# Kernel optimization log

Measured on AMD Instinct MI355X. Metric: run time of the kernel, lower is better.

## Reference

```python
import jax, jax.numpy as jnp
import numpy as np

D_K = 64
MASK_FILL = -1e9


def setup_inputs() -> dict:
    key = jax.random.key(0)
    kq, kk, kv, km = jax.random.split(key, 4)
    B, H, S, D = 2, 16, 2048, D_K
    q = jax.random.normal(kq, (B, H, S, D), dtype=jnp.float32)
    k = jax.random.normal(kk, (B, H, D, S), dtype=jnp.float32)  # pre-transposed keys
    v = jax.random.normal(kv, (B, H, S, D), dtype=jnp.float32)
    mask = jax.random.randint(km, (B, H, S, S), 0, 2).astype(jnp.bool_)
    return {"q": q, "k": k, "v": v, "mask": mask}


def reference(q, k, v, mask):
    # scores: [B, H, S, S] = q @ k (k already [B,H,D,S])
    scores = jnp.einsum("bhsd,bhdt->bhst", q, k) / jnp.sqrt(jnp.float32(D_K))
    scores = jnp.where(mask, MASK_FILL, scores)
    attn = jax.nn.softmax(scores, axis=-1)
    context = jnp.einsum("bhst,bhtd->bhsd", attn, v)
    return (context, attn)
```

## Files before the change

### kernel.cpp

```cpp
#include <hip/hip_runtime.h>

#define S_LEN    2048
#define DK       64
#define N_BH     32
#define ROWS     16
#define NTHREADS 512

typedef float          f32x4  __attribute__((ext_vector_type(4)));
typedef int            i32x4  __attribute__((ext_vector_type(4)));
typedef short          bf16x8 __attribute__((ext_vector_type(8)));
typedef unsigned short u16x8  __attribute__((ext_vector_type(8)));
typedef unsigned int   u32x4  __attribute__((ext_vector_type(4)));

__device__ __forceinline__ unsigned short f2bf(float f) {
    unsigned u = __builtin_bit_cast(unsigned, f);
    u += 0x7fffu + ((u >> 16) & 1u);
    return (unsigned short)(u >> 16);
}
__device__ __forceinline__ float bf2f(unsigned short h) {
    unsigned u = ((unsigned)h) << 16;
    return __builtin_bit_cast(float, u);
}
__device__ __forceinline__ unsigned pack_bf2(float a, float b) {
    return (unsigned)f2bf(a) | ((unsigned)f2bf(b) << 16);
}

__global__ void prep_qcast(const float* __restrict__ q, unsigned short* __restrict__ Qb) {
    const long i = ((long)blockIdx.x * 256 + threadIdx.x) * 8;
    f32x4 a = *(const f32x4*)(q + i);
    f32x4 b = *(const f32x4*)(q + i + 4);
    u16x8 o;
    o[0]=f2bf(a.x); o[1]=f2bf(a.y); o[2]=f2bf(a.z); o[3]=f2bf(a.w);
    o[4]=f2bf(b.x); o[5]=f2bf(b.y); o[6]=f2bf(b.z); o[7]=f2bf(b.w);
    *(u16x8*)(Qb + i) = o;
}

__global__ void prep_k(const float* __restrict__ k, unsigned short* __restrict__ Kb) {
    __shared__ float t[64][65];
    const int bh = blockIdx.x >> 5, s0 = (blockIdx.x & 31) << 6;
    const int tx = threadIdx.x;
    const float* kb = k + (long)bh * 64 * S_LEN;
    #pragma unroll
    for (int i = 0; i < 16; ++i) {
        const int d = (i << 2) + (tx >> 6), s = tx & 63;
        t[d][s] = kb[(long)d * S_LEN + s0 + s];
    }
    __syncthreads();
    #pragma unroll
    for (int i = 0; i < 16; ++i) {
        const int s = (i << 2) + (tx >> 6), d = tx & 63;
        Kb[((long)bh * S_LEN + s0 + s) * DK + d] = f2bf(t[d][s]);
    }
}

__global__ void prep_v(const float* __restrict__ v, unsigned short* __restrict__ Vb) {
    __shared__ float t[64][65];
    const int bh = blockIdx.x >> 5, s0 = (blockIdx.x & 31) << 6;
    const int tx = threadIdx.x;
    #pragma unroll
    for (int i = 0; i < 16; ++i) {
        const int s = (i << 2) + (tx >> 6), d = tx & 63;
        t[s][d] = v[((long)bh * S_LEN + s0 + s) * DK + d];
    }
    __syncthreads();
    #pragma unroll
    for (int i = 0; i < 16; ++i) {
        const int d = (i << 2) + (tx >> 6), s = tx & 63;
        Vb[((long)bh * DK + d) * S_LEN + s0 + s] = f2bf(t[s][d]);
    }
}

template <bool WS>
__global__ __launch_bounds__(NTHREADS, 4)
void sdpa_main(const float* __restrict__ q, const float* __restrict__ k,
               const float* __restrict__ v, const int* __restrict__ mask,
               const unsigned short* __restrict__ Qb,
               const unsigned short* __restrict__ Kb,
               const unsigned short* __restrict__ Vb,
               float* __restrict__ ctx, float* __restrict__ attn)
{
    __shared__ float rowsum[ROWS];
    __shared__ float ctxlds[ROWS * DK];

    const int bid  = blockIdx.x;
    const int bh   = bid & (N_BH - 1);
    const int qt   = bid >> 5;
    const int tid  = threadIdx.x;
    const int wave = tid >> 6;
    const int lane = tid & 63;
    const int m    = lane & 15;
    const int g    = lane >> 4;
    const long rowbase = (long)bh * S_LEN + qt * ROWS;
    const int tw   = wave << 8;

    if (tid < ROWS) rowsum[tid] = 0.0f;
    for (int i = tid; i < ROWS * DK; i += NTHREADS) ctxlds[i] = 0.0f;
    __syncthreads();

    unsigned long long mbits = 0ull;
    {
        const int* mbase = mask + rowbase * S_LEN + tw + 4 * lane;
        #pragma unroll
        for (int r = 0; r < 16; ++r) {
            const i32x4 mk = __builtin_nontemporal_load((const i32x4*)(mbase + (long)r * S_LEN));
            const unsigned nib = (mk.x ? 1u : 0u) | (mk.y ? 2u : 0u)
                               | (mk.z ? 4u : 0u) | (mk.w ? 8u : 0u);
            mbits |= ((unsigned long long)nib) << (r * 4);
        }
    }

    bf16x8 qfrag[2];
    if (WS) {
        const unsigned short* qp = Qb + (rowbase + m) * DK;
        qfrag[0] = *(const bf16x8*)(qp + g * 8);
        qfrag[1] = *(const bf16x8*)(qp + 32 + g * 8);
    } else {
        const float* qp = q + (rowbase + m) * DK;
        #pragma unroll
        for (int ks = 0; ks < 2; ++ks) {
            const float* p = qp + ks * 32 + g * 8;
            f32x4 x0 = *(const f32x4*)p, x1 = *(const f32x4*)(p + 4);
            qfrag[ks][0]=(short)f2bf(x0.x); qfrag[ks][1]=(short)f2bf(x0.y);
            qfrag[ks][2]=(short)f2bf(x0.z); qfrag[ks][3]=(short)f2bf(x0.w);
            qfrag[ks][4]=(short)f2bf(x1.x); qfrag[ks][5]=(short)f2bf(x1.y);
            qfrag[ks][6]=(short)f2bf(x1.z); qfrag[ks][7]=(short)f2bf(x1.w);
        }
    }

    unsigned long long lanemask = 0ull;
    {
        const unsigned mlo = (unsigned)mbits, mhi = (unsigned)(mbits >> 32);
        #pragma unroll
        for (int kt = 0; kt < 8; ++kt) {
            const int sA = kt * 8 + g * 2, sB = sA + 1;
            const unsigned aLo = (unsigned)__shfl((int)mlo, sA);
            const unsigned aHi = (unsigned)__shfl((int)mhi, sA);
            const unsigned bLo = (unsigned)__shfl((int)mlo, sB);
            const unsigned bHi = (unsigned)__shfl((int)mhi, sB);
            const unsigned long long A = ((unsigned long long)aHi << 32) | aLo;
            const unsigned long long B = ((unsigned long long)bHi << 32) | bLo;
            const unsigned byt = (unsigned)((A >> (4 * m)) & 0xFull)
                               | ((unsigned)((B >> (4 * m)) & 0xFull) << 4);
            lanemask |= ((unsigned long long)byt) << (8 * kt);
        }
    }

    const int srcA = ((g & 1) << 5) + m;
    const int srcB = srcA + 16;
    const int hi   = g >> 1;

    u32x4 AF[8];
    f32x4 cacc0 = {0,0,0,0}, cacc1 = {0,0,0,0}, cacc2 = {0,0,0,0}, cacc3 = {0,0,0,0};
    float rsum = 0.0f;

    #pragma unroll
    for (int kt = 0; kt < 8; ++kt) {
        unsigned pk0e, pk1e, pk0o, pk1o;
        #pragma unroll
        for (int h = 0; h < 2; ++h) {
            const int t0 = tw + ((2 * kt + h) << 4);
            const int tk = t0 + m;
            f32x4 acc = {0.f, 0.f, 0.f, 0.f};
            #pragma unroll
            for (int ks = 0; ks < 2; ++ks) {
                bf16x8 kfrag;
                if (WS) {
                    kfrag = *(const bf16x8*)(Kb + ((long)bh * S_LEN + tk) * DK + ks * 32 + g * 8);
                } else {
                    const float* kp = k + (long)bh * DK * S_LEN + (long)(ks * 32 + g * 8) * S_LEN + tk;
                    #pragma unroll
                    for (int j = 0; j < 8; ++j) kfrag[j] = (short)f2bf(kp[(long)j * S_LEN]);
                }
                acc = __builtin_amdgcn_mfma_f32_16x16x32_bf16(kfrag, qfrag[ks], acc, 0, 0, 0);
            }
            const float e0 = __expf(acc[0] * 0.125f);
            const float e1 = __expf(acc[1] * 0.125f);
            const float e2 = __expf(acc[2] * 0.125f);
            const float e3 = __expf(acc[3] * 0.125f);
            if (h == 0) { pk0e = pack_bf2(e0, e1); pk1e = pack_bf2(e2, e3); }
            else        { pk0o = pack_bf2(e0, e1); pk1o = pack_bf2(e2, e3); }
        }
        const unsigned a0e = (unsigned)__shfl((int)pk0e, srcA);
        const unsigned a0o = (unsigned)__shfl((int)pk0o, srcA);
        const unsigned a1e = (unsigned)__shfl((int)pk1e, srcA);
        const unsigned a1o = (unsigned)__shfl((int)pk1o, srcA);
        const unsigned a2e = (unsigned)__shfl((int)pk0e, srcB);
        const unsigned a2o = (unsigned)__shfl((int)pk0o, srcB);
        const unsigned a3e = (unsigned)__shfl((int)pk1e, srcB);
        const unsigned a3o = (unsigned)__shfl((int)pk1o, srcB);
        u32x4 wv = { hi ? a0o : a0e, hi ? a1o : a1e,
                     hi ? a2o : a2e, hi ? a3o : a3e };
        const unsigned mb = (unsigned)(lanemask >> (8 * kt)) & 0xFFu;
        if (mb & 1u)   wv.x &= 0xFFFF0000u;
        if (mb & 2u)   wv.x &= 0x0000FFFFu;
        if (mb & 4u)   wv.y &= 0xFFFF0000u;
        if (mb & 8u)   wv.y &= 0x0000FFFFu;
        if (mb & 16u)  wv.z &= 0xFFFF0000u;
        if (mb & 32u)  wv.z &= 0x0000FFFFu;
        if (mb & 64u)  wv.w &= 0xFFFF0000u;
        if (mb & 128u) wv.w &= 0x0000FFFFu;
        AF[kt] = wv;
        rsum += ((bf2f((unsigned short)(wv.x & 0xFFFF)) + bf2f((unsigned short)(wv.x >> 16)))
               + (bf2f((unsigned short)(wv.y & 0xFFFF)) + bf2f((unsigned short)(wv.y >> 16))))
              + ((bf2f((unsigned short)(wv.z & 0xFFFF)) + bf2f((unsigned short)(wv.z >> 16)))
               + (bf2f((unsigned short)(wv.w & 0xFFFF)) + bf2f((unsigned short)(wv.w >> 16))));
        const bf16x8 af = __builtin_bit_cast(bf16x8, wv);
        const int tb = tw + (kt << 5) + (g << 3);
        #pragma unroll
        for (int dt = 0; dt < 4; ++dt) {
            bf16x8 bfv;
            if (WS) {
                bfv = *(const bf16x8*)(Vb + ((long)bh * DK + dt * 16 + m) * S_LEN + tb);
            } else {
                const float* vp = v + ((long)bh * S_LEN + tb) * DK + dt * 16 + m;
                #pragma unroll
                for (int j = 0; j < 8; ++j) bfv[j] = (short)f2bf(vp[j * DK]);
            }
            if      (dt == 0) cacc0 = __builtin_amdgcn_mfma_f32_16x16x32_bf16(af, bfv, cacc0, 0, 0, 0);
            else if (dt == 1) cacc1 = __builtin_amdgcn_mfma_f32_16x16x32_bf16(af, bfv, cacc1, 0, 0, 0);
            else if (dt == 2) cacc2 = __builtin_amdgcn_mfma_f32_16x16x32_bf16(af, bfv, cacc2, 0, 0, 0);
            else              cacc3 = __builtin_amdgcn_mfma_f32_16x16x32_bf16(af, bfv, cacc3, 0, 0, 0);
        }
    }

    rsum += __shfl_xor(rsum, 16);
    rsum += __shfl_xor(rsum, 32);
    if (lane < 16) atomicAdd(&rowsum[lane], rsum);
    #pragma unroll
    for (int i = 0; i < 4; ++i) {
        atomicAdd(&ctxlds[(4 * g + i) * DK +  0 + m], cacc0[i]);
        atomicAdd(&ctxlds[(4 * g + i) * DK + 16 + m], cacc1[i]);
        atomicAdd(&ctxlds[(4 * g + i) * DK + 32 + m], cacc2[i]);
        atomicAdd(&ctxlds[(4 * g + i) * DK + 48 + m], cacc3[i]);
    }
    __syncthreads();

    {
        const float rinv = 1.0f / rowsum[m];
        float* aout = attn + (rowbase + m) * (long)S_LEN;
        #pragma unroll
        for (int kt = 0; kt < 8; ++kt) {
            const u32x4 wv = AF[kt];
            const int tb = tw + (kt << 5) + (g << 3);
            f32x4 o0 = { bf2f((unsigned short)(wv.x & 0xFFFF)) * rinv,
                         bf2f((unsigned short)(wv.x >> 16))    * rinv,
                         bf2f((unsigned short)(wv.y & 0xFFFF)) * rinv,
                         bf2f((unsigned short)(wv.y >> 16))    * rinv };
            f32x4 o1 = { bf2f((unsigned short)(wv.z & 0xFFFF)) * rinv,
                         bf2f((unsigned short)(wv.z >> 16))    * rinv,
                         bf2f((unsigned short)(wv.w & 0xFFFF)) * rinv,
                         bf2f((unsigned short)(wv.w >> 16))    * rinv };
            __builtin_nontemporal_store(o0, (f32x4*)(aout + tb));
            __builtin_nontemporal_store(o1, (f32x4*)(aout + tb + 4));
        }
    }

    #pragma unroll
    for (int i = tid; i < ROWS * DK; i += NTHREADS) {
        const int rr = i >> 6, dd = i & 63;
        ctx[(rowbase + rr) * DK + dd] = ctxlds[i] / rowsum[rr];
    }
}

extern "C" void kernel_launch(void* const* d_in, const int* in_sizes, int n_in,
                              void* d_out, int out_size, void* d_ws, size_t ws_size,
                              hipStream_t stream)
{
    const float* q    = (const float*)d_in[0];
    const float* k    = (const float*)d_in[1];
    const float* v    = (const float*)d_in[2];
    const int*   mask = (const int*)d_in[3];

    float* ctx  = (float*)d_out;
    float* attn = ctx + (size_t)N_BH * S_LEN * DK;

    const size_t nel = (size_t)N_BH * S_LEN * DK;
    const bool use_ws = ws_size >= nel * 3 * sizeof(unsigned short);
    unsigned short* Qb = (unsigned short*)d_ws;
    unsigned short* Kb = Qb + nel;
    unsigned short* Vb = Kb + nel;

    const int nblocks = N_BH * (S_LEN / ROWS);

    if (use_ws) {
        prep_qcast<<<(int)(nel / (256 * 8)), 256, 0, stream>>>(q, Qb);
        prep_k<<<N_BH * (S_LEN / 64), 256, 0, stream>>>(k, Kb);
        prep_v<<<N_BH * (S_LEN / 64), 256, 0, stream>>>(v, Vb);
        sdpa_main<true><<<nblocks, NTHREADS, 0, stream>>>(q, k, v, mask, Qb, Kb, Vb, ctx, attn);
    } else {
        sdpa_main<false><<<nblocks, NTHREADS, 0, stream>>>(q, k, v, mask,
                                                           nullptr, nullptr, nullptr, ctx, attn);
    }
}
```

Baseline: 475.9 us.

## Pre-swizzle Q/K/V bf16 into MFMA fragment order for contiguous wave loads

The prep kernels now write the bf16 copies of Q, K and V in the exact per-lane fragment order the MFMA instructions consume, so each wave's fragment load becomes one contiguous 1 KB read (lane*8 offset). Before, the main kernel used strided row loads, and the V^T layout was read with an S_LEN stride. This targets memory coalescing and address arithmetic in the main attention loop. The prep kernels get more complex, with vectorised 16-byte stores built from gathered LDS reads.

```diff
diff --git a/kernel.cpp b/kernel.cpp
--- a/kernel.cpp
+++ b/kernel.cpp
@@ -25,21 +25,24 @@
     return (unsigned)f2bf(a) | ((unsigned)f2bf(b) << 16);
 }
 
-__global__ void prep_qcast(const float* __restrict__ q, unsigned short* __restrict__ Qb) {
-    const long i = ((long)blockIdx.x * 256 + threadIdx.x) * 8;
-    f32x4 a = *(const f32x4*)(q + i);
-    f32x4 b = *(const f32x4*)(q + i + 4);
+__global__ void prep_q(const float* __restrict__ q, unsigned short* __restrict__ Q2) {
+    const int bq = blockIdx.x;
+    const int tx = threadIdx.x;
+    const int ks = tx >> 6, g = (tx >> 4) & 3, m = tx & 15;
+    const long row = ((long)(bq >> 7) * S_LEN + (bq & 127) * 16 + m);
+    const float* p = q + row * DK + ks * 32 + g * 8;
+    f32x4 x0 = *(const f32x4*)p, x1 = *(const f32x4*)(p + 4);
     u16x8 o;
-    o[0]=f2bf(a.x); o[1]=f2bf(a.y); o[2]=f2bf(a.z); o[3]=f2bf(a.w);
-    o[4]=f2bf(b.x); o[5]=f2bf(b.y); o[6]=f2bf(b.z); o[7]=f2bf(b.w);
-    *(u16x8*)(Qb + i) = o;
-}
-
-__global__ void prep_k(const float* __restrict__ k, unsigned short* __restrict__ Kb) {
+    o[0]=f2bf(x0.x); o[1]=f2bf(x0.y); o[2]=f2bf(x0.z); o[3]=f2bf(x0.w);
+    o[4]=f2bf(x1.x); o[5]=f2bf(x1.y); o[6]=f2bf(x1.z); o[7]=f2bf(x1.w);
+    *(u16x8*)(Q2 + (long)bq * 1024 + tx * 8) = o;
+}
+
+__global__ void prep_k(const float* __restrict__ k, unsigned short* __restrict__ K2) {
     __shared__ float t[64][65];
     const int bh = blockIdx.x >> 5, s0 = (blockIdx.x & 31) << 6;
     const int tx = threadIdx.x;
-    const float* kb = k + (long)bh * 64 * S_LEN;
+    const float* kb = k + (long)bh * DK * S_LEN;
     #pragma unroll
     for (int i = 0; i < 16; ++i) {
         const int d = (i << 2) + (tx >> 6), s = tx & 63;
@@ -47,13 +50,20 @@
     }
     __syncthreads();
     #pragma unroll
-    for (int i = 0; i < 16; ++i) {
-        const int s = (i << 2) + (tx >> 6), d = tx & 63;
-        Kb[((long)bh * S_LEN + s0 + s) * DK + d] = f2bf(t[d][s]);
-    }
-}
-
-__global__ void prep_v(const float* __restrict__ v, unsigned short* __restrict__ Vb) {
+    for (int it = 0; it < 2; ++it) {
+        const int flat = it * 256 + tx;
+        const int m = flat & 15, g = (flat >> 4) & 3, ks = (flat >> 6) & 1, t16g = flat >> 7;
+        const int sl = t16g * 16 + m;
+        const int d0 = ks * 32 + g * 8;
+        u16x8 o;
+        #pragma unroll
+        for (int j = 0; j < 8; ++j) o[j] = f2bf(t[d0 + j][sl]);
+        const long idx = ((((long)(bh * 128 + (s0 >> 4) + t16g) * 2 + ks) * 4 + g) * 16 + m) * 8;
+        *(u16x8*)(K2 + idx) = o;
+    }
+}
+
+__global__ void prep_v(const float* __restrict__ v, unsigned short* __restrict__ V2) {
     __shared__ float t[64][65];
     const int bh = blockIdx.x >> 5, s0 = (blockIdx.x & 31) << 6;
     const int tx = threadIdx.x;
@@ -64,9 +74,14 @@
     }
     __syncthreads();
     #pragma unroll
-    for (int i = 0; i < 16; ++i) {
-        const int d = (i << 2) + (tx >> 6), s = tx & 63;
-        Vb[((long)bh * DK + d) * S_LEN + s0 + s] = f2bf(t[s][d]);
+    for (int it = 0; it < 2; ++it) {
+        const int flat = it * 256 + tx;
+        const int d = flat & 63, tbl = flat >> 6;
+        u16x8 o;
+        #pragma unroll
+        for (int j = 0; j < 8; ++j) o[j] = f2bf(t[tbl * 8 + j][d]);
+        const long idx = (((long)(bh * 256 + (s0 >> 3) + tbl) * 64) + d) * 8;
+        *(u16x8*)(V2 + idx) = o;
     }
 }
 
@@ -74,9 +89,9 @@
 __global__ __launch_bounds__(NTHREADS, 4)
 void sdpa_main(const float* __restrict__ q, const float* __restrict__ k,
                const float* __restrict__ v, const int* __restrict__ mask,
-               const unsigned short* __restrict__ Qb,
-               const unsigned short* __restrict__ Kb,
-               const unsigned short* __restrict__ Vb,
+               const unsigned short* __restrict__ Q2,
+               const unsigned short* __restrict__ K2,
+               const unsigned short* __restrict__ V2,
                float* __restrict__ ctx, float* __restrict__ attn)
 {
     __shared__ float rowsum[ROWS];
@@ -111,9 +126,9 @@
 
     bf16x8 qfrag[2];
     if (WS) {
-        const unsigned short* qp = Qb + (rowbase + m) * DK;
-        qfrag[0] = *(const bf16x8*)(qp + g * 8);
-        qfrag[1] = *(const bf16x8*)(qp + 32 + g * 8);
+        const unsigned short* qp = Q2 + ((long)((bh * 128 + qt) * 2) << 9) + (lane << 3);
+        qfrag[0] = *(const bf16x8*)qp;
+        qfrag[1] = *(const bf16x8*)(qp + 512);
     } else {
         const float* qp = q + (rowbase + m) * DK;
         #pragma unroll
@@ -158,15 +173,18 @@
         unsigned pk0e, pk1e, pk0o, pk1o;
         #pragma unroll
         for (int h = 0; h < 2; ++h) {
-            const int t0 = tw + ((2 * kt + h) << 4);
-            const int tk = t0 + m;
             f32x4 acc = {0.f, 0.f, 0.f, 0.f};
             #pragma unroll
             for (int ks = 0; ks < 2; ++ks) {
                 bf16x8 kfrag;
                 if (WS) {
-                    kfrag = *(const bf16x8*)(Kb + ((long)bh * S_LEN + tk) * DK + ks * 32 + g * 8);
+                    const unsigned short* kp = K2
+                        + (((long)(bh * 128 + wave * 16 + 2 * kt + h) * 2 + ks) << 9)
+                        + (lane << 3);
+                    kfrag = *(const bf16x8*)kp;
                 } else {
+                    const int t0 = tw + ((2 * kt + h) << 4);
+                    const int tk = t0 + m;
                     const float* kp = k + (long)bh * DK * S_LEN + (long)(ks * 32 + g * 8) * S_LEN + tk;
                     #pragma unroll
                     for (int j = 0; j < 8; ++j) kfrag[j] = (short)f2bf(kp[(long)j * S_LEN]);
@@ -205,13 +223,15 @@
               + ((bf2f((unsigned short)(wv.z & 0xFFFF)) + bf2f((unsigned short)(wv.z >> 16)))
                + (bf2f((unsigned short)(wv.w & 0xFFFF)) + bf2f((unsigned short)(wv.w >> 16))));
         const bf16x8 af = __builtin_bit_cast(bf16x8, wv);
-        const int tb = tw + (kt << 5) + (g << 3);
         #pragma unroll
         for (int dt = 0; dt < 4; ++dt) {
             bf16x8 bfv;
             if (WS) {
-                bfv = *(const bf16x8*)(Vb + ((long)bh * DK + dt * 16 + m) * S_LEN + tb);
+                const unsigned short* vp2 = V2
+                    + ((((long)(bh * 256 + (wave << 5) + (kt << 2) + g)) << 6) + dt * 16 + m) * 8;
+                bfv = *(const bf16x8*)vp2;
             } else {
+                const int tb = tw + (kt << 5) + (g << 3);
                 const float* vp = v + ((long)bh * S_LEN + tb) * DK + dt * 16 + m;
                 #pragma unroll
                 for (int j = 0; j < 8; ++j) bfv[j] = (short)f2bf(vp[j * DK]);
@@ -276,17 +296,17 @@
 
     const size_t nel = (size_t)N_BH * S_LEN * DK;
     const bool use_ws = ws_size >= nel * 3 * sizeof(unsigned short);
-    unsigned short* Qb = (unsigned short*)d_ws;
-    unsigned short* Kb = Qb + nel;
-    unsigned short* Vb = Kb + nel;
+    unsigned short* Q2 = (unsigned short*)d_ws;
+    unsigned short* K2 = Q2 + nel;
+    unsigned short* V2 = K2 + nel;
 
     const int nblocks = N_BH * (S_LEN / ROWS);
 
     if (use_ws) {
-        prep_qcast<<<(int)(nel / (256 * 8)), 256, 0, stream>>>(q, Qb);
-        prep_k<<<N_BH * (S_LEN / 64), 256, 0, stream>>>(k, Kb);
-        prep_v<<<N_BH * (S_LEN / 64), 256, 0, stream>>>(v, Vb);
-        sdpa_main<true><<<nblocks, NTHREADS, 0, stream>>>(q, k, v, mask, Qb, Kb, Vb, ctx, attn);
+        prep_q<<<N_BH * 128, 128, 0, stream>>>(q, Q2);
+        prep_k<<<N_BH * (S_LEN / 64), 256, 0, stream>>>(k, K2);
+        prep_v<<<N_BH * (S_LEN / 64), 256, 0, stream>>>(v, V2);
+        sdpa_main<true><<<nblocks, NTHREADS, 0, stream>>>(q, k, v, mask, Q2, K2, V2, ctx, attn);
     } else {
         sdpa_main<false><<<nblocks, NTHREADS, 0, stream>>>(q, k, v, mask,
                                                            nullptr, nullptr, nullptr, ctx, attn);
```

After: 459.1 us. -3.5%, faster.
